# Kernel optimization log

Hardware: AMD Instinct MI355X
Metric: run time of the kernel (lower is better)

The kernel has to match this reference:

```python
import jax, jax.numpy as jnp
import numpy as np
import math

BINSIZE = 200
WIDTH = 100000
BINWIDTH = WIDTH // BINSIZE  # 500
WINDOW0 = 0


def setup_inputs() -> dict:
    key = jax.random.key(0)
    ks = jax.random.split(key, 8)
    n_regions, n_clusters = 5000, 20
    n_regions_oi, n_fragments, n_cells = 200, 2_000_000, 100_000
    return {
        "baseline_weight": jax.random.normal(ks[0], (n_regions, BINWIDTH), dtype=jnp.float32),
        "delta_logit_weight": jax.random.normal(ks[1], (n_regions, n_clusters, BINWIDTH), dtype=jnp.float32),
        "inside": jnp.ones((1,), dtype=jnp.float32),
        "regions_oi": jax.random.randint(ks[2], (n_regions_oi,), 0, n_regions),
        "coordinates": jax.random.randint(ks[3], (n_fragments, 2), 0, WIDTH),
        "local_region_ix": jax.random.randint(ks[4], (n_fragments,), 0, n_regions_oi),
        "local_cell_ix": jax.random.randint(ks[5], (n_fragments,), 0, n_cells),
        "labels": jax.random.randint(ks[6], (n_cells,), 0, n_clusters),
    }


def reference(baseline_weight, delta_logit_weight, inside, regions_oi,
              coordinates, local_region_ix, local_cell_ix, labels):
    # Embedding lookups: [R_oi, 1, B] + [R_oi, C, B]
    unnormalized = baseline_weight[regions_oi][:, None, :] + delta_logit_weight[regions_oi]
    # log-softmax over bins, converted to density (divide by binsize)
    heights = jax.nn.log_softmax(unnormalized, axis=-1) - math.log(BINSIZE)
    # bin indices for left/right coordinates
    bin_left = (coordinates[:, 0] - WINDOW0) // BINSIZE
    bin_right = (coordinates[:, 1] - WINDOW0) // BINSIZE
    # triple-indexed gather: (region, cluster-of-cell, bin) -> scalar logprob
    logprob_left = heights[local_region_ix, labels[local_cell_ix], bin_left]
    # inside/outside term for the right coordinate
    match = (bin_left == bin_right).astype(heights.dtype)  # [N]
    s = jax.nn.sigmoid(inside)  # [1]
    logprob_inside = jnp.log(s) - math.log(BINWIDTH)
    logprob_outside = jnp.log(1.0 - s) - math.log(WIDTH - BINWIDTH)
    logprob_right = logprob_inside * match + logprob_outside * (1.0 - match)  # [N]
    return jnp.stack([logprob_left, logprob_right], axis=-1)  # [N, 2]
```

## Files before the change

### kernel.cpp

```cpp
#include <hip/hip_runtime.h>
#include <hip/hip_bf16.h>
#include <hip/hip_fp16.h>
#include <math.h>
#include <string.h>

#define BINSIZE 200
#define BINW 500
#define NCLUST 20
#define NREG_OI 200
#define LOG_BINSIZE   5.2983173665480363f
#define LOG_BINWIDTH  6.2146080984221914f
#define LOG_OUTWIDTH 11.5079131920500050f

typedef int   vint2   __attribute__((ext_vector_type(2)));
typedef int   vint4   __attribute__((ext_vector_type(4)));
typedef float vfloat4 __attribute__((ext_vector_type(4)));

__global__ void heights_kernel(const float* __restrict__ baseline,
                               const float* __restrict__ delta,
                               const int*   __restrict__ regions_oi,
                               _Float16*    __restrict__ heights)
{
    const int wave = blockIdx.x * 4 + (threadIdx.x >> 6);
    const int lane = threadIdx.x & 63;
    if (wave >= NREG_OI * NCLUST) return;

    const int r = wave / NCLUST;
    const int c = wave % NCLUST;
    const int g = regions_oi[r];

    const float* bptr = baseline + (size_t)g * BINW;
    const float* dptr = delta + ((size_t)g * NCLUST + c) * BINW;

    float u[8];
    float m = -INFINITY;
#pragma unroll
    for (int k = 0; k < 8; ++k) {
        const int b = lane + 64 * k;
        u[k] = (b < BINW)
             ? (bptr[b] + __builtin_nontemporal_load(dptr + b))
             : -INFINITY;
        m = fmaxf(m, u[k]);
    }
#pragma unroll
    for (int off = 32; off > 0; off >>= 1)
        m = fmaxf(m, __shfl_xor(m, off));

    float s = 0.f;
#pragma unroll
    for (int k = 0; k < 8; ++k) {
        const int b = lane + 64 * k;
        if (b < BINW) s += __expf(u[k] - m);
    }
#pragma unroll
    for (int off = 32; off > 0; off >>= 1)
        s += __shfl_xor(s, off);

    const float lse = m + __logf(s);
    _Float16* hptr = heights + (size_t)wave * BINW;
#pragma unroll
    for (int k = 0; k < 8; ++k) {
        const int b = lane + 64 * k;
        if (b < BINW) hptr[b] = (_Float16)(u[k] - lse - LOG_BINSIZE);
    }
}

__global__ __launch_bounds__(256)
void frag_kernel(const _Float16* __restrict__ heights,
                 const int*      __restrict__ coords,
                 const int*      __restrict__ lrix,
                 const int*      __restrict__ lcix,
                 const int*      __restrict__ labels,
                 const float*    __restrict__ inside,
                 float*          __restrict__ out,
                 int N)
{
    const int q  = blockIdx.x * blockDim.x + threadIdx.x;
    const int f0 = q * 4;
    if (f0 >= N) return;

    const float x  = inside[0];
    const float sg = 1.f / (1.f + __expf(-x));
    const float lp_in  = __logf(sg)       - LOG_BINWIDTH;
    const float lp_out = __logf(1.f - sg) - LOG_OUTWIDTH;

    if (f0 + 3 < N) {
        const vint4 c01 = __builtin_nontemporal_load((const vint4*)coords + 2 * q);
        const vint4 c23 = __builtin_nontemporal_load((const vint4*)coords + 2 * q + 1);
        const vint4 rr  = __builtin_nontemporal_load((const vint4*)lrix + q);
        const vint4 ce  = __builtin_nontemporal_load((const vint4*)lcix + q);

        const int lab0 = labels[ce.x];
        const int lab1 = labels[ce.y];
        const int lab2 = labels[ce.z];
        const int lab3 = labels[ce.w];

        const unsigned bl0 = (unsigned)c01.x / (unsigned)BINSIZE;
        const unsigned br0 = (unsigned)c01.y / (unsigned)BINSIZE;
        const unsigned bl1 = (unsigned)c01.z / (unsigned)BINSIZE;
        const unsigned br1 = (unsigned)c01.w / (unsigned)BINSIZE;
        const unsigned bl2 = (unsigned)c23.x / (unsigned)BINSIZE;
        const unsigned br2 = (unsigned)c23.y / (unsigned)BINSIZE;
        const unsigned bl3 = (unsigned)c23.z / (unsigned)BINSIZE;
        const unsigned br3 = (unsigned)c23.w / (unsigned)BINSIZE;

        const float h0 = (float)heights[((size_t)rr.x * NCLUST + lab0) * BINW + bl0];
        const float h1 = (float)heights[((size_t)rr.y * NCLUST + lab1) * BINW + bl1];
        const float h2 = (float)heights[((size_t)rr.z * NCLUST + lab2) * BINW + bl2];
        const float h3 = (float)heights[((size_t)rr.w * NCLUST + lab3) * BINW + bl3];

        vfloat4 o01, o23;
        o01.x = h0;
        o01.y = (bl0 == br0) ? lp_in : lp_out;
        o01.z = h1;
        o01.w = (bl1 == br1) ? lp_in : lp_out;
        o23.x = h2;
        o23.y = (bl2 == br2) ? lp_in : lp_out;
        o23.z = h3;
        o23.w = (bl3 == br3) ? lp_in : lp_out;
        __builtin_nontemporal_store(o01, (vfloat4*)out + 2 * q);
        __builtin_nontemporal_store(o23, (vfloat4*)out + 2 * q + 1);
    } else {
        for (int f = f0; f < N; ++f) {
            const unsigned bl = (unsigned)coords[2 * f]     / (unsigned)BINSIZE;
            const unsigned br = (unsigned)coords[2 * f + 1] / (unsigned)BINSIZE;
            const int lab = labels[lcix[f]];
            const float h = (float)heights[((size_t)lrix[f] * NCLUST + lab) * BINW + bl];
            out[2 * f]     = h;
            out[2 * f + 1] = (bl == br) ? lp_in : lp_out;
        }
    }
}

extern "C" void kernel_launch(void* const* d_in, const int* in_sizes, int n_in,
                              void* d_out, int out_size, void* d_ws, size_t ws_size,
                              hipStream_t stream) {
    const float* baseline   = (const float*)d_in[0];
    const float* delta      = (const float*)d_in[1];
    const float* inside     = (const float*)d_in[2];
    const int*   regions_oi = (const int*)d_in[3];
    const int*   coords     = (const int*)d_in[4];
    const int*   lrix       = (const int*)d_in[5];
    const int*   lcix       = (const int*)d_in[6];
    const int*   labels     = (const int*)d_in[7];
    float*       out        = (float*)d_out;
    _Float16*    heights    = (_Float16*)d_ws;

    const int N     = in_sizes[4] / 2;
    const int Nquad = (N + 3) / 4;

    heights_kernel<<<(NREG_OI * NCLUST + 3) / 4, 256, 0, stream>>>(
        baseline, delta, regions_oi, heights);

    frag_kernel<<<(Nquad + 255) / 256, 256, 0, stream>>>(
        heights, coords, lrix, lcix, labels, inside, out, N);
}
```

Before: 285.9 us.

## Pack labels to bytes in heights kernel and process eight fragments per thread

The heights kernel gains extra blocks that compress the int32 cluster labels into a byte array in workspace, so the per-fragment label gather in the fragment kernel reads a 100KB table instead of 400KB. That table is more likely to stay cache-resident. The fragment kernel now handles eight fragments per thread with wider vector loads, which raises memory-level parallelism per thread. Index arithmetic is switched from size_t to int. The costs are more registers per thread, fewer threads in flight, and a workspace offset fixed at 4MB.

```diff
diff --git a/kernel.cpp b/kernel.cpp
--- a/kernel.cpp
+++ b/kernel.cpp
@@ -12,15 +12,38 @@
 #define LOG_BINWIDTH  6.2146080984221914f
 #define LOG_OUTWIDTH 11.5079131920500050f
 
+
 typedef int   vint2   __attribute__((ext_vector_type(2)));
 typedef int   vint4   __attribute__((ext_vector_type(4)));
 typedef float vfloat4 __attribute__((ext_vector_type(4)));
 
+#define HBLOCKS 1000
+#define LBLOCKS 98
+
 __global__ void heights_kernel(const float* __restrict__ baseline,
                                const float* __restrict__ delta,
                                const int*   __restrict__ regions_oi,
-                               _Float16*    __restrict__ heights)
+                               const int*   __restrict__ labels,
+                               _Float16*    __restrict__ heights,
+                               unsigned char* __restrict__ labels8,
+                               int ncells)
 {
+    if (blockIdx.x >= HBLOCKS) {
+        const int t = (blockIdx.x - HBLOCKS) * 256 + threadIdx.x;
+        const int i0 = t * 4;
+        if (i0 + 3 < ncells) {
+            const vint4 l = __builtin_nontemporal_load((const vint4*)labels + t);
+            unsigned packed = (unsigned)(l.x & 0xff)
+                            | ((unsigned)(l.y & 0xff) << 8)
+                            | ((unsigned)(l.z & 0xff) << 16)
+                            | ((unsigned)(l.w & 0xff) << 24);
+            *(unsigned*)(labels8 + i0) = packed;
+        } else {
+            for (int i = i0; i < ncells; ++i) labels8[i] = (unsigned char)labels[i];
+        }
+        return;
+    }
+
     const int wave = blockIdx.x * 4 + (threadIdx.x >> 6);
     const int lane = threadIdx.x & 63;
     if (wave >= NREG_OI * NCLUST) return;
@@ -67,16 +90,16 @@
 
 __global__ __launch_bounds__(256)
 void frag_kernel(const _Float16* __restrict__ heights,
+                 const unsigned char* __restrict__ labels8,
                  const int*      __restrict__ coords,
                  const int*      __restrict__ lrix,
                  const int*      __restrict__ lcix,
-                 const int*      __restrict__ labels,
                  const float*    __restrict__ inside,
                  float*          __restrict__ out,
                  int N)
 {
     const int q  = blockIdx.x * blockDim.x + threadIdx.x;
-    const int f0 = q * 4;
+    const int f0 = q * 8;
     if (f0 >= N) return;
 
     const float x  = inside[0];
@@ -84,48 +107,54 @@
     const float lp_in  = __logf(sg)       - LOG_BINWIDTH;
     const float lp_out = __logf(1.f - sg) - LOG_OUTWIDTH;
 
-    if (f0 + 3 < N) {
-        const vint4 c01 = __builtin_nontemporal_load((const vint4*)coords + 2 * q);
-        const vint4 c23 = __builtin_nontemporal_load((const vint4*)coords + 2 * q + 1);
-        const vint4 rr  = __builtin_nontemporal_load((const vint4*)lrix + q);
-        const vint4 ce  = __builtin_nontemporal_load((const vint4*)lcix + q);
+    if (f0 + 7 < N) {
+        vint4 cc[4];
+#pragma unroll
+        for (int j = 0; j < 4; ++j)
+            cc[j] = __builtin_nontemporal_load((const vint4*)coords + 4 * q + j);
+        const vint4 r0 = __builtin_nontemporal_load((const vint4*)lrix + 2 * q);
+        const vint4 r1 = __builtin_nontemporal_load((const vint4*)lrix + 2 * q + 1);
+        const vint4 e0 = __builtin_nontemporal_load((const vint4*)lcix + 2 * q);
+        const vint4 e1 = __builtin_nontemporal_load((const vint4*)lcix + 2 * q + 1);
 
-        const int lab0 = labels[ce.x];
-        const int lab1 = labels[ce.y];
-        const int lab2 = labels[ce.z];
-        const int lab3 = labels[ce.w];
+        const int rr[8] = { r0.x, r0.y, r0.z, r0.w, r1.x, r1.y, r1.z, r1.w };
+        const int ce[8] = { e0.x, e0.y, e0.z, e0.w, e1.x, e1.y, e1.z, e1.w };
 
-        const unsigned bl0 = (unsigned)c01.x / (unsigned)BINSIZE;
-        const unsigned br0 = (unsigned)c01.y / (unsigned)BINSIZE;
-        const unsigned bl1 = (unsigned)c01.z / (unsigned)BINSIZE;
-        const unsigned br1 = (unsigned)c01.w / (unsigned)BINSIZE;
-        const unsigned bl2 = (unsigned)c23.x / (unsigned)BINSIZE;
-        const unsigned br2 = (unsigned)c23.y / (unsigned)BINSIZE;
-        const unsigned bl3 = (unsigned)c23.z / (unsigned)BINSIZE;
-        const unsigned br3 = (unsigned)c23.w / (unsigned)BINSIZE;
+        int lab[8];
+#pragma unroll
+        for (int k = 0; k < 8; ++k) lab[k] = (int)labels8[ce[k]];
 
-        const float h0 = (float)heights[((size_t)rr.x * NCLUST + lab0) * BINW + bl0];
-        const float h1 = (float)heights[((size_t)rr.y * NCLUST + lab1) * BINW + bl1];
-        const float h2 = (float)heights[((size_t)rr.z * NCLUST + lab2) * BINW + bl2];
-        const float h3 = (float)heights[((size_t)rr.w * NCLUST + lab3) * BINW + bl3];
+        unsigned bl[8], br[8];
+#pragma unroll
+        for (int j = 0; j < 4; ++j) {
+            bl[2 * j]     = (unsigned)cc[j].x / (unsigned)BINSIZE;
+            br[2 * j]     = (unsigned)cc[j].y / (unsigned)BINSIZE;
+            bl[2 * j + 1] = (unsigned)cc[j].z / (unsigned)BINSIZE;
+            br[2 * j + 1] = (unsigned)cc[j].w / (unsigned)BINSIZE;
+        }
 
-        vfloat4 o01, o23;
-        o01.x = h0;
-        o01.y = (bl0 == br0) ? lp_in : lp_out;
-        o01.z = h1;
-        o01.w = (bl1 == br1) ? lp_in : lp_out;
-        o23.x = h2;
-        o23.y = (bl2 == br2) ? lp_in : lp_out;
-        o23.z = h3;
-        o23.w = (bl3 == br3) ? lp_in : lp_out;
-        __builtin_nontemporal_store(o01, (vfloat4*)out + 2 * q);
-        __builtin_nontemporal_store(o23, (vfloat4*)out + 2 * q + 1);
+        float h[8];
+#pragma unroll
+        for (int k = 0; k < 8; ++k) {
+            const int idx = (rr[k] * NCLUST + lab[k]) * BINW + (int)bl[k];
+            h[k] = (float)heights[idx];
+        }
+
+#pragma unroll
+        for (int j = 0; j < 4; ++j) {
+            vfloat4 o;
+            o.x = h[2 * j];
+            o.y = (bl[2 * j]     == br[2 * j])     ? lp_in : lp_out;
+            o.z = h[2 * j + 1];
+            o.w = (bl[2 * j + 1] == br[2 * j + 1]) ? lp_in : lp_out;
+            __builtin_nontemporal_store(o, (vfloat4*)out + 4 * q + j);
+        }
     } else {
         for (int f = f0; f < N; ++f) {
             const unsigned bl = (unsigned)coords[2 * f]     / (unsigned)BINSIZE;
             const unsigned br = (unsigned)coords[2 * f + 1] / (unsigned)BINSIZE;
-            const int lab = labels[lcix[f]];
-            const float h = (float)heights[((size_t)lrix[f] * NCLUST + lab) * BINW + bl];
+            const int lab = (int)labels8[lcix[f]];
+            const float h = (float)heights[(lrix[f] * NCLUST + lab) * BINW + (int)bl];
             out[2 * f]     = h;
             out[2 * f + 1] = (bl == br) ? lp_in : lp_out;
         }
@@ -144,14 +173,17 @@
     const int*   lcix       = (const int*)d_in[6];
     const int*   labels     = (const int*)d_in[7];
     float*       out        = (float*)d_out;
-    _Float16*    heights    = (_Float16*)d_ws;
 
-    const int N     = in_sizes[4] / 2;
-    const int Nquad = (N + 3) / 4;
+    _Float16*      heights = (_Float16*)d_ws;
+    unsigned char* labels8 = (unsigned char*)d_ws + (4u << 20);
 
-    heights_kernel<<<(NREG_OI * NCLUST + 3) / 4, 256, 0, stream>>>(
-        baseline, delta, regions_oi, heights);
+    const int N      = in_sizes[4] / 2;
+    const int ncells = in_sizes[7];
+    const int Noct   = (N + 7) / 8;
 
-    frag_kernel<<<(Nquad + 255) / 256, 256, 0, stream>>>(
-        heights, coords, lrix, lcix, labels, inside, out, N);
+    heights_kernel<<<HBLOCKS + LBLOCKS, 256, 0, stream>>>(
+        baseline, delta, regions_oi, labels, heights, labels8, ncells);
+
+    frag_kernel<<<(Noct + 255) / 256, 256, 0, stream>>>(
+        heights, labels8, coords, lrix, lcix, inside, out, N);
 }
```

New measurement: 283.0 us. About the same (-1.0%).
